# Kernel optimization log

Hardware: AMD Instinct MI355X
Metric: run time of the kernel (lower is better)

The kernel has to match this reference:

```python
import jax, jax.numpy as jnp
import numpy as np

D, K, B, IMG, NCH = 128, 512, 8, 128, 3


def adder2d(x, w, k, stride, pad):
    # AdderNet L1 'convolution': y[b,co,l] = -sum_p |patch[b,p,l] - w[co,p]|
    # x: [B,C,H,W], w: [Cout, C*k*k]
    p = jax.lax.conv_general_dilated_patches(x, (k, k), (stride, stride), [(pad, pad), (pad, pad)])
    Bb, P, Ho, Wo = p.shape
    p = p.reshape(Bb, P, Ho * Wo)  # [B, C*k*k, L]
    def one(wc):  # wc: [P] -> [B, L]; sequential over Cout to bound memory
        return -jnp.sum(jnp.abs(p - wc[None, :, None]), axis=1)
    o = jax.lax.map(one, w)  # [Cout, B, L]
    return jnp.transpose(o, (1, 0, 2)).reshape(Bb, w.shape[0], Ho, Wo)


def bn(x, g, b, eps=1e-5):
    # eval-mode BatchNorm2d with running_mean=0, running_var=1
    s = g * jax.lax.rsqrt(jnp.asarray(1.0 + eps, x.dtype))
    return x * s[None, :, None, None] + b[None, :, None, None]


def conv2d(x, w, b, pad):
    y = jax.lax.conv_general_dilated(x, w, (1, 1), [(pad, pad), (pad, pad)],
                                     dimension_numbers=('NCHW', 'OIHW', 'NCHW'))
    return y + b[None, :, None, None]


def up2x(x):  # nn.Upsample(scale_factor=2, bilinear, align_corners=False)
    Bb, C, H, W = x.shape
    return jax.image.resize(x, (Bb, C, 2 * H, 2 * W), method='bilinear')


def adder_resblock(x, w1, w2, g, b):
    # [ReLU, adder3x3, BN, ReLU, adder1x1] + residual
    h = jax.nn.relu(x)
    h = adder2d(h, w1, 3, 1, 1)
    h = bn(h, g, b)
    h = jax.nn.relu(h)
    h = adder2d(h, w2, 1, 1, 0)
    return x + h


def conv_resblock(x, w1, b1, w2, b2):
    # [ReLU, conv3x3, ReLU, conv1x1] + residual (bn=False in decoder)
    h = jax.nn.relu(x)
    h = conv2d(h, w1, b1, 1)
    h = jax.nn.relu(h)
    h = conv2d(h, w2, b2, 0)
    return x + h


def vq_forward(z_e, E):
    # NearestEmbed: E is [d, k]
    Bb, C, H, W = z_e.shape
    flat = jnp.transpose(z_e, (0, 2, 3, 1)).reshape(-1, C)  # [N, d]
    d2 = (jnp.sum(flat * flat, axis=1, keepdims=True)
          - 2.0 * (flat @ E) + jnp.sum(E * E, axis=0)[None, :])  # [N, k]
    argmin = jnp.argmin(d2, axis=1)  # [N]
    q = jnp.take(E.T, argmin, axis=0)  # [N, d]
    # weight_sg=True path: straight-through to z_e, no grad to E
    zq_flat = flat + jax.lax.stop_gradient(q - flat)
    z_q = jnp.transpose(zq_flat.reshape(Bb, H, W, C), (0, 3, 1, 2))
    # emb path: z_e detached, grad flows to E through the gather
    emb = jnp.transpose(q.reshape(Bb, H, W, C), (0, 3, 1, 2))
    return z_q, emb, argmin.reshape(Bb, H, W)


def reference(x, we1, we2, ae1_w1, ae1_w2, ae2_w1, ae2_w2, bn_gamma, bn_beta,
              emb_weight, rd1_w1, rd1_b1, rd1_w2, rd1_b2, rd2_w1, rd2_b1,
              rd2_w2, rd2_b2, cd1_w, cd1_b, cd2_w, cd2_b):
    g, b = bn_gamma, bn_beta
    h = adder2d(x, we1, 4, 2, 1)
    h = jax.nn.relu(bn(h, g[0], b[0]))
    h = adder2d(h, we2, 4, 2, 1)
    h = jax.nn.relu(bn(h, g[1], b[1]))
    h = adder_resblock(h, ae1_w1, ae1_w2, g[2], b[2])
    h = bn(h, g[3], b[3])
    h = adder_resblock(h, ae2_w1, ae2_w2, g[4], b[4])
    z_e = bn(h, g[5], b[5])  # bne4 (gamma = 1/40)

    z_q, emb, argmin = vq_forward(z_e, emb_weight)

    y = conv_resblock(z_q, rd1_w1, rd1_b1, rd1_w2, rd1_b2)
    y = bn(y, g[6], b[6])
    y = conv_resblock(y, rd2_w1, rd2_b1, rd2_w2, rd2_b2)
    y = up2x(y)
    y = conv2d(y, cd1_w, cd1_b, 1)
    y = jax.nn.relu(bn(y, g[7], b[7]))
    y = up2x(y)
    y = conv2d(y, cd2_w, cd2_b, 1)
    y = jnp.tanh(y)
    return (y, z_e, emb, argmin)


def setup_inputs() -> dict:
    key = jax.random.key(0)
    ks = jax.random.split(key, 16)
    f = lambda k, shp: (0.02 * jax.random.normal(k, shp)).astype(jnp.float32)
    inp = {}
    inp['x'] = jax.random.normal(ks[0], (B, NCH, IMG, IMG), jnp.float32)
    inp['we1'] = f(ks[1], (D, NCH * 16))       # adder 4x4 s2
    inp['we2'] = f(ks[2], (D, D * 16))
    inp['ae1_w1'] = f(ks[3], (D, D * 9))       # adder 3x3
    inp['ae1_w2'] = f(ks[4], (D, D))           # adder 1x1
    inp['ae2_w1'] = f(ks[5], (D, D * 9))
    inp['ae2_w2'] = f(ks[6], (D, D))
    inp['bn_gamma'] = jnp.ones((8, D), jnp.float32).at[5].set(1.0 / 40.0)
    inp['bn_beta'] = jnp.zeros((8, D), jnp.float32)
    inp['emb_weight'] = f(ks[7], (D, K))
    inp['rd1_w1'] = f(ks[8], (D, D, 3, 3)); inp['rd1_b1'] = jnp.zeros(D, jnp.float32)
    inp['rd1_w2'] = f(ks[9], (D, D, 1, 1)); inp['rd1_b2'] = jnp.zeros(D, jnp.float32)
    inp['rd2_w1'] = f(ks[10], (D, D, 3, 3)); inp['rd2_b1'] = jnp.zeros(D, jnp.float32)
    inp['rd2_w2'] = f(ks[11], (D, D, 1, 1)); inp['rd2_b2'] = jnp.zeros(D, jnp.float32)
    inp['cd1_w'] = f(ks[12], (D, D, 3, 3)); inp['cd1_b'] = jnp.zeros(D, jnp.float32)
    inp['cd2_w'] = f(ks[13], (NCH, D, 3, 3)); inp['cd2_b'] = jnp.zeros(NCH, jnp.float32)
    return inp
```

## Files before the change

kernel.cpp:

```cpp
#include <hip/hip_runtime.h>
#include <math.h>

constexpr int Dc = 128;
constexpr int Kc = 512;
constexpr int Bc = 8;

template<int ISADD, int K, int STRIDE, int PAD, int IT, int EPI, int CIN, int CH,
         int PW, int OUT_ROWS, int WOUT, int WIN, int HIN, int HOUT, int COBW,
         int NW, int KSPLIT>
__global__ __launch_bounds__(NW * 64)
void lds_layer(const float* __restrict__ x, const float* __restrict__ w,
               const float* __restrict__ bias,
               const float* __restrict__ itG, const float* __restrict__ itB,
               const float* __restrict__ res,
               const float* __restrict__ rG, const float* __restrict__ rB,
               const float* __restrict__ oG, const float* __restrict__ oB,
               float* __restrict__ out) {
  constexpr int BT = NW * 64;
  constexpr int NWG = NW / KSPLIT;
  constexpr int CINW = CIN / KSPLIT;
  constexpr int CHS = KSPLIT * CH;
  constexpr int KK = K * K;
  constexpr int SPAN = (PW - 1) * STRIDE + K;
  constexpr int IN_ROWS = (OUT_ROWS - 1) * STRIDE + K;
  constexpr int WPAD = (WOUT - 1) * STRIDE + K;
  constexpr int WLDS = (WPAD + 3) & ~3;
  constexpr int PGW = WOUT / PW;
  static_assert(OUT_ROWS * PGW == 64, "one wave covers the pixel tile");
  static_assert(NW % KSPLIT == 0 && CIN % KSPLIT == 0 && CINW % CH == 0, "split");
  static_assert(KSPLIT == 1 ||
                NWG * 64 * PW * COBW <= CHS * IN_ROWS * WLDS, "scratch fits");
  constexpr int NBAND = HOUT / OUT_ROWS;
  constexpr int W4 = WIN / 4;
  constexpr int NELEM4 = CHS * IN_ROWS * W4;
  constexpr int NIT4 = (NELEM4 + BT - 1) / BT;
  constexpr bool EXACT = (NELEM4 % BT) == 0;
  const float r15 = rsqrtf(1.0f + 1e-5f);

  __shared__ alignas(16) float lds[CHS][IN_ROWS][WLDS];

  int tid = threadIdx.x;
  int gb = blockIdx.x;
  int cg = gb / (Bc * NBAND);
  int rem = gb % (Bc * NBAND);
  int band = rem % NBAND;
  int b = rem / NBAND;
  int wv = __builtin_amdgcn_readfirstlane(tid >> 6);
  int lane = tid & 63;
  int grp = wv / NWG;
  int wloc = wv % NWG;
  int co0 = cg * (NWG * COBW) + wloc * COBW;
  int pr = lane / PGW, pc = lane % PGW;
  int oh = band * OUT_ROWS + pr;
  int ow0 = pc * PW;
  int yi0 = band * OUT_ROWS * STRIDE - PAD;

  for (int e = tid; e < CHS * IN_ROWS * WLDS; e += BT) ((float*)lds)[e] = 0.f;

  float acc[PW][COBW];
#pragma unroll
  for (int p = 0; p < PW; ++p)
#pragma unroll
    for (int j = 0; j < COBW; ++j)
      acc[p][j] = (ISADD || grp != 0) ? 0.f : bias[co0 + j];

  const float* xb = x + (long)b * CIN * HIN * WIN;
  float4 rbuf[NIT4];

  auto stage = [&](int cc) {
#pragma unroll
    for (int it = 0; it < NIT4; ++it) {
      int e = it * BT + tid;
      if (!EXACT && e >= NELEM4) break;
      int c4 = e % W4;
      int r = (e / W4) % IN_ROWS;
      int ch2 = e / (W4 * IN_ROWS);
      int gc = cc + (ch2 % CH) + (ch2 / CH) * CINW;
      int yi = yi0 + r;
      float4 v = make_float4(0.f, 0.f, 0.f, 0.f);
      if (yi >= 0 && yi < HIN) {
        v = *(const float4*)&xb[((long)gc * HIN + yi) * WIN + 4 * c4];
        if (IT == 1) {
          v.x = fmaxf(v.x, 0.f); v.y = fmaxf(v.y, 0.f);
          v.z = fmaxf(v.z, 0.f); v.w = fmaxf(v.w, 0.f);
        }
        if (IT == 2) {
          float sc = itG[gc] * r15, bc = itB[gc];
          v.x = fmaxf(fmaf(v.x, sc, bc), 0.f);
          v.y = fmaxf(fmaf(v.y, sc, bc), 0.f);
          v.z = fmaxf(fmaf(v.z, sc, bc), 0.f);
          v.w = fmaxf(fmaf(v.w, sc, bc), 0.f);
        }
      }
      rbuf[it] = v;
    }
  };
  auto towrite = [&]() {
#pragma unroll
    for (int it = 0; it < NIT4; ++it) {
      int e = it * BT + tid;
      if (!EXACT && e >= NELEM4) break;
      int c4 = e % W4;
      int r = (e / W4) % IN_ROWS;
      int ch2 = e / (W4 * IN_ROWS);
      float* p = &lds[ch2][r][4 * c4 + PAD];
      float4 v = rbuf[it];
      p[0] = v.x; p[1] = v.y; p[2] = v.z; p[3] = v.w;
    }
  };

  stage(0);
  for (int cc = 0; cc < CINW; cc += CH) {
    __syncthreads();
    towrite();
    __syncthreads();
    if (cc + CH < CINW) stage(cc + CH);
    for (int chl = 0; chl < CH; ++chl) {
      float vbuf[K][SPAN];
#pragma unroll
      for (int kh = 0; kh < K; ++kh) {
        const float* rp0 = &lds[grp * CH + chl][pr * STRIDE + kh][ow0 * STRIDE];
        if constexpr (SPAN == 6 && (PW * STRIDE) % 4 == 0) {
          float4 a = *(const float4*)rp0;
          float2 c2 = *(const float2*)(rp0 + 4);
          vbuf[kh][0] = a.x; vbuf[kh][1] = a.y; vbuf[kh][2] = a.z;
          vbuf[kh][3] = a.w; vbuf[kh][4] = c2.x; vbuf[kh][5] = c2.y;
        } else if constexpr (SPAN == 4 && (PW * STRIDE) % 2 == 0) {
          float2 a = *(const float2*)rp0;
          float2 c2 = *(const float2*)(rp0 + 2);
          vbuf[kh][0] = a.x; vbuf[kh][1] = a.y;
          vbuf[kh][2] = c2.x; vbuf[kh][3] = c2.y;
        } else if constexpr (SPAN == 2 && (PW * STRIDE) % 2 == 0) {
          float2 a = *(const float2*)rp0;
          vbuf[kh][0] = a.x; vbuf[kh][1] = a.y;
        } else {
#pragma unroll
          for (int s = 0; s < SPAN; ++s) vbuf[kh][s] = rp0[s];
        }
      }
      const float* wc = w + ((long)co0 * CIN + (grp * CINW + cc + chl)) * KK;
#pragma unroll
      for (int kh = 0; kh < K; ++kh)
#pragma unroll
        for (int kw = 0; kw < K; ++kw)
#pragma unroll
          for (int j = 0; j < COBW; ++j) {
            float ww = wc[(long)j * CIN * KK + kh * K + kw];
#pragma unroll
            for (int p = 0; p < PW; ++p) {
              float v = vbuf[kh][p * STRIDE + kw];
              if (ISADD) acc[p][j] += fabsf(v - ww);
              else       acc[p][j] = fmaf(v, ww, acc[p][j]);
            }
          }
    }
  }

  if constexpr (KSPLIT >= 2) {
    float* scr = (float*)lds;
    int sb = (wloc * 64 + lane) * (PW * COBW);
#pragma unroll
    for (int g = 1; g < KSPLIT; ++g) {
      __syncthreads();
      if (grp == g) {
#pragma unroll
        for (int p = 0; p < PW; ++p)
#pragma unroll
          for (int j = 0; j < COBW; ++j) scr[sb + p * COBW + j] = acc[p][j];
      }
      __syncthreads();
      if (grp == 0) {
#pragma unroll
        for (int p = 0; p < PW; ++p)
#pragma unroll
          for (int j = 0; j < COBW; ++j) acc[p][j] += scr[sb + p * COBW + j];
      }
    }
    if (grp != 0) return;
  }

  long obase = ((long)(b * Dc + co0) * HOUT + oh) * WOUT + ow0;
  float* ob = out + obase;
  const float* rp = (EPI == 2 || EPI == 3 || EPI == 6) ? res + obase : nullptr;
  constexpr long hw = (long)HOUT * WOUT;
#pragma unroll
  for (int j = 0; j < COBW; ++j) {
    float og = 0.f, obb = 0.f, rg = 0.f, rbb = 0.f;
    if (EPI == 1 || EPI == 6) { og = oG[co0 + j] * r15; obb = oB[co0 + j]; }
    if (EPI == 3 || EPI == 6) { rg = rG[co0 + j] * r15; rbb = rB[co0 + j]; }
#pragma unroll
    for (int p = 0; p < PW; ++p) {
      float val = ISADD ? -acc[p][j] : acc[p][j];
      if (EPI == 1) val = fmaxf(fmaf(val, og, obb), 0.f);
      if (EPI == 2) val = rp[j * hw + p] + val;
      if (EPI == 3) val = fmaf(rp[j * hw + p], rg, rbb) + val;
      if (EPI == 5) val = fmaxf(val, 0.f);
      if (EPI == 6) val = fmaf(fmaf(rp[j * hw + p], rg, rbb) + val, og, obb);
      ob[j * hw + p] = val;
    }
  }
}

template<int ISADD, int EPI, int COBW>
__global__ __launch_bounds__(256)
void pw1x1(const float* __restrict__ x, const float* __restrict__ w,
           const float* __restrict__ bias,
           const float* __restrict__ res,
           const float* __restrict__ rG, const float* __restrict__ rB,
           const float* __restrict__ oG, const float* __restrict__ oB,
           float* __restrict__ out) {
  constexpr int HW = 1024;
  constexpr int CIN = Dc;
  constexpr int KS = 4;
  constexpr int CSEG = CIN / KS;
  constexpr int PXB = 128;
  constexpr int NPG = HW / PXB;
  constexpr int OPT = (PXB * COBW) / 256;
  static_assert(OPT * 256 == PXB * COBW, "combine exact");
  const float r15 = rsqrtf(1.0f + 1e-5f);

  __shared__ float scr[KS][COBW][PXB];

  int tid = threadIdx.x;
  int wv = __builtin_amdgcn_readfirstlane(tid >> 6);
  int lane = tid & 63;
  int gb = blockIdx.x;
  int cg = gb / (Bc * NPG);
  int rem = gb % (Bc * NPG);
  int pg = rem % NPG;
  int b = rem / NPG;
  int co0 = cg * COBW;
  int px = pg * PXB + lane * 2;

  const float* xc = x + ((long)b * CIN + wv * CSEG) * HW + px;
  const float* wseg = w + wv * CSEG;

  float acc[2][COBW];
#pragma unroll
  for (int p = 0; p < 2; ++p)
#pragma unroll
    for (int j = 0; j < COBW; ++j) acc[p][j] = 0.f;

#pragma unroll 4
  for (int c = 0; c < CSEG; ++c) {
    float2 v = *(const float2*)&xc[(long)c * HW];
#pragma unroll
    for (int j = 0; j < COBW; ++j) {
      float ww = wseg[(long)(co0 + j) * CIN + c];
      if (ISADD) {
        acc[0][j] += fabsf(v.x - ww);
        acc[1][j] += fabsf(v.y - ww);
      } else {
        acc[0][j] = fmaf(v.x, ww, acc[0][j]);
        acc[1][j] = fmaf(v.y, ww, acc[1][j]);
      }
    }
  }

#pragma unroll
  for (int j = 0; j < COBW; ++j) {
    float2 t = make_float2(acc[0][j], acc[1][j]);
    *(float2*)&scr[wv][j][lane * 2] = t;
  }
  __syncthreads();

#pragma unroll
  for (int k = 0; k < OPT; ++k) {
    int e = k * 256 + tid;
    int pxl = e % PXB;
    int j = e / PXB;
    float s = scr[0][j][pxl] + scr[1][j][pxl] + scr[2][j][pxl] + scr[3][j][pxl];
    float val = ISADD ? -s : s + bias[co0 + j];
    long oidx = ((long)b * Dc + co0 + j) * HW + pg * PXB + pxl;
    if (EPI == 2) val = res[oidx] + val;
    if (EPI == 3) {
      float rg = rG[co0 + j] * r15, rbb = rB[co0 + j];
      val = fmaf(res[oidx], rg, rbb) + val;
    }
    if (EPI == 6) {
      float rg = rG[co0 + j] * r15, rbb = rB[co0 + j];
      float og = oG[co0 + j] * r15, obb = oB[co0 + j];
      val = fmaf(fmaf(res[oidx], rg, rbb) + val, og, obb);
    }
    out[oidx] = val;
  }
}

__device__ __forceinline__ void up_coef(int p, int H, int& i0, int& i1, float& w0, float& w1) {
  int m = p >> 1;
  if ((p & 1) == 0) { i0 = (m > 0) ? m - 1 : 0; i1 = m; w0 = 0.25f; w1 = 0.75f; }
  else              { i0 = m; i1 = (m + 1 < H) ? m + 1 : H - 1; w0 = 0.75f; w1 = 0.25f; }
}

__global__ void up2x_kernel(const float* __restrict__ in, float* __restrict__ out,
                            int C, int H, int W) {
  int H2 = 2 * H, W2 = 2 * W;
  int i = blockIdx.x * blockDim.x + threadIdx.x;
  int total = Bc * C * H2 * W2;
  if (i >= total) return;
  int ow = i % W2; int t = i / W2;
  int oh = t % H2; t /= H2;
  int c = t % C; int b = t / C;
  int y0, y1, x0, x1; float wy0, wy1, wx0, wx1;
  up_coef(oh, H, y0, y1, wy0, wy1);
  up_coef(ow, W, x0, x1, wx0, wx1);
  const float* p = in + (b * C + c) * H * W;
  float v = wy0 * (wx0 * p[y0 * W + x0] + wx1 * p[y0 * W + x1])
          + wy1 * (wx0 * p[y1 * W + x0] + wx1 * p[y1 * W + x1]);
  out[i] = v;
}

__global__ __launch_bounds__(256)
void conv3x3_up_tanh_quad(const float* __restrict__ x, const float* __restrict__ w,
                          const float* __restrict__ bias, float* __restrict__ out,
                          int Hs, int Ws, int Cout) {
  constexpr int CIN = Dc;
  int H2 = 2 * Hs, W2 = 2 * Ws;
  int nq = Hs * Ws;
  int i = blockIdx.x * blockDim.x + threadIdx.x;
  int total = Bc * Cout * nq;
  if (i >= total) return;
  int q = i % nq; int t = i / nq;
  int co = t % Cout; int b = t / Cout;
  int n = q % Ws, m = q / Ws;
  int rows[3] = { (m > 0) ? m - 1 : 0, m, (m + 1 < Hs) ? m + 1 : Hs - 1 };
  int cols[3] = { (n > 0) ? n - 1 : 0, n, (n + 1 < Ws) ? n + 1 : Ws - 1 };
  float rv[4] = { (2 * m - 1 >= 0) ? 1.f : 0.f, 1.f, 1.f, (2 * m + 2 < H2) ? 1.f : 0.f };
  float cv[4] = { (2 * n - 1 >= 0) ? 1.f : 0.f, 1.f, 1.f, (2 * n + 2 < W2) ? 1.f : 0.f };
  float bco = bias[co];
  float acc[4] = { bco, bco, bco, bco };
  const float* xb = x + b * CIN * nq;
  const float* wb = w + co * CIN * 9;
  for (int c = 0; c < CIN; ++c) {
    const float* xc = xb + c * nq;
    float s[3][3];
#pragma unroll
    for (int a = 0; a < 3; ++a)
#pragma unroll
      for (int e = 0; e < 3; ++e) s[a][e] = xc[rows[a] * Ws + cols[e]];
    float rb[4][3];
#pragma unroll
    for (int e = 0; e < 3; ++e) {
      rb[0][e] = fmaf(0.75f, s[0][e], 0.25f * s[1][e]);
      rb[1][e] = fmaf(0.25f, s[0][e], 0.75f * s[1][e]);
      rb[2][e] = fmaf(0.75f, s[1][e], 0.25f * s[2][e]);
      rb[3][e] = fmaf(0.25f, s[1][e], 0.75f * s[2][e]);
    }
    float u[4][4];
#pragma unroll
    for (int di = 0; di < 4; ++di) {
      float rm = rv[di];
      u[di][0] = fmaf(0.75f, rb[di][0], 0.25f * rb[di][1]) * rm * cv[0];
      u[di][1] = fmaf(0.25f, rb[di][0], 0.75f * rb[di][1]) * rm * cv[1];
      u[di][2] = fmaf(0.75f, rb[di][1], 0.25f * rb[di][2]) * rm * cv[2];
      u[di][3] = fmaf(0.25f, rb[di][1], 0.75f * rb[di][2]) * rm * cv[3];
    }
    const float* wc = wb + c * 9;
#pragma unroll
    for (int kh = 0; kh < 3; ++kh)
#pragma unroll
      for (int kw = 0; kw < 3; ++kw) {
        float ww = wc[kh * 3 + kw];
        acc[0] = fmaf(u[kh][kw],         ww, acc[0]);
        acc[1] = fmaf(u[kh][kw + 1],     ww, acc[1]);
        acc[2] = fmaf(u[kh + 1][kw],     ww, acc[2]);
        acc[3] = fmaf(u[kh + 1][kw + 1], ww, acc[3]);
      }
  }
  float* ob = out + (b * Cout + co) * H2 * W2 + (2 * m) * W2 + 2 * n;
  ob[0] = tanhf(acc[0]);      ob[1] = tanhf(acc[1]);
  ob[W2] = tanhf(acc[2]);     ob[W2 + 1] = tanhf(acc[3]);
}

__global__ __launch_bounds__(256)
void vq_kernel8(const float* __restrict__ z_e, const float* __restrict__ E,
                float* __restrict__ emb, float* __restrict__ argmin_out) {
  constexpr int HW = 1024;
  __shared__ alignas(16) float f[8][Dc];
  __shared__ float d2s[8][256];
  __shared__ int   ks[8][256];
  int tid = threadIdx.x;
  int n0 = blockIdx.x * 8;
  int b = n0 >> 10;
  int rem = n0 & 1023;
  const float* zb = z_e + (long)b * Dc * HW + rem;
#pragma unroll
  for (int i = 0; i < 4; ++i) {
    int e = i * 256 + tid;
    int p = e & 7, d = e >> 3;
    f[p][d] = zb[d * HW + p];
  }
  __syncthreads();
  float f2 = 0.f;
  if (tid < 8) {
    for (int d = 0; d < Dc; ++d) f2 += f[tid][d] * f[tid][d];
    d2s[tid][0] = f2;
  }
  __syncthreads();
  float f2v[8];
#pragma unroll
  for (int p = 0; p < 8; ++p) f2v[p] = d2s[p][0];
  __syncthreads();

  float best[8]; int bk[8];
#pragma unroll
  for (int p = 0; p < 8; ++p) { best[p] = 3.4e38f; bk[p] = 0; }
  for (int kk = tid; kk < Kc; kk += 256) {
    float dot[8];
#pragma unroll
    for (int p = 0; p < 8; ++p) dot[p] = 0.f;
    float e2k = 0.f;
    for (int d4 = 0; d4 < Dc; d4 += 4) {
      float e0 = E[(long)(d4 + 0) * Kc + kk];
      float e1 = E[(long)(d4 + 1) * Kc + kk];
      float e2c = E[(long)(d4 + 2) * Kc + kk];
      float e3 = E[(long)(d4 + 3) * Kc + kk];
      e2k = fmaf(e0, e0, e2k);
      e2k = fmaf(e1, e1, e2k);
      e2k = fmaf(e2c, e2c, e2k);
      e2k = fmaf(e3, e3, e2k);
#pragma unroll
      for (int p = 0; p < 8; ++p) {
        float4 fv = *(const float4*)&f[p][d4];
        dot[p] = fmaf(fv.x, e0, dot[p]);
        dot[p] = fmaf(fv.y, e1, dot[p]);
        dot[p] = fmaf(fv.z, e2c, dot[p]);
        dot[p] = fmaf(fv.w, e3, dot[p]);
      }
    }
#pragma unroll
    for (int p = 0; p < 8; ++p) {
      float d2 = f2v[p] - 2.f * dot[p] + e2k;
      if (d2 < best[p] || (d2 == best[p] && kk < bk[p])) { best[p] = d2; bk[p] = kk; }
    }
  }
#pragma unroll
  for (int p = 0; p < 8; ++p) { d2s[p][tid] = best[p]; ks[p][tid] = bk[p]; }
  __syncthreads();
  for (int s = 128; s > 0; s >>= 1) {
    if (tid < s) {
#pragma unroll
      for (int p = 0; p < 8; ++p) {
        float ob = d2s[p][tid + s]; int ok = ks[p][tid + s];
        if (ob < d2s[p][tid] || (ob == d2s[p][tid] && ok < ks[p][tid])) {
          d2s[p][tid] = ob; ks[p][tid] = ok;
        }
      }
    }
    __syncthreads();
  }
  if (tid < 8) argmin_out[n0 + tid] = (float)ks[tid][0];
  float* eb = emb + (long)b * Dc * HW + rem;
#pragma unroll
  for (int i = 0; i < 4; ++i) {
    int e = i * 256 + tid;
    int p = e & 7, d = e >> 3;
    eb[d * HW + p] = E[d * Kc + ks[p][0]];
  }
}

extern "C" void kernel_launch(void* const* d_in, const int* in_sizes, int n_in,
                              void* d_out, int out_size, void* d_ws, size_t ws_size,
                              hipStream_t stream) {
  const float* x      = (const float*)d_in[0];
  const float* we1    = (const float*)d_in[1];
  const float* we2    = (const float*)d_in[2];
  const float* ae1_w1 = (const float*)d_in[3];
  const float* ae1_w2 = (const float*)d_in[4];
  const float* ae2_w1 = (const float*)d_in[5];
  const float* ae2_w2 = (const float*)d_in[6];
  const float* bn_g   = (const float*)d_in[7];
  const float* bn_b   = (const float*)d_in[8];
  const float* embw   = (const float*)d_in[9];
  const float* rd1_w1 = (const float*)d_in[10];
  const float* rd1_b1 = (const float*)d_in[11];
  const float* rd1_w2 = (const float*)d_in[12];
  const float* rd1_b2 = (const float*)d_in[13];
  const float* rd2_w1 = (const float*)d_in[14];
  const float* rd2_b1 = (const float*)d_in[15];
  const float* rd2_w2 = (const float*)d_in[16];
  const float* rd2_b2 = (const float*)d_in[17];
  const float* cd1_w  = (const float*)d_in[18];
  const float* cd1_b  = (const float*)d_in[19];
  const float* cd2_w  = (const float*)d_in[20];
  const float* cd2_b  = (const float*)d_in[21];

  const float* g0 = bn_g + 0 * Dc; const float* b0 = bn_b + 0 * Dc;
  const float* g1 = bn_g + 1 * Dc; const float* b1 = bn_b + 1 * Dc;
  const float* g2 = bn_g + 2 * Dc; const float* b2 = bn_b + 2 * Dc;
  const float* g3 = bn_g + 3 * Dc; const float* b3 = bn_b + 3 * Dc;
  const float* g4 = bn_g + 4 * Dc; const float* b4 = bn_b + 4 * Dc;
  const float* g5 = bn_g + 5 * Dc; const float* b5 = bn_b + 5 * Dc;
  const float* g6 = bn_g + 6 * Dc; const float* b6 = bn_b + 6 * Dc;
  const float* g7 = bn_g + 7 * Dc; const float* b7 = bn_b + 7 * Dc;

  float* W64a = (float*)d_ws;
  float* W64b = W64a + 4194304;
  float* Wa   = W64b + 4194304;
  float* Wb   = Wa + 1048576;
  float* Wc   = Wb + 1048576;

  float* out_y   = (float*)d_out;
  float* out_ze  = out_y  + 393216;
  float* out_emb = out_ze + 1048576;
  float* out_am  = out_emb + 1048576;

  const int TB = 256;
  const int TB8 = 512;
  auto nb = [](int n) { return (n + 255) / 256; };
  const int N64 = Bc * Dc * 64 * 64;
  const float* nul = nullptr;

  const int G32s = 16 * Bc * 8;
  const int Gwe1 = 8 * Bc * 32;
  const int Gcd1 = 4 * Bc * 32;
  const int Gpw  = 32 * Bc * 8;

  lds_layer<1,4,2,1, 0,1, 3,3, 2, 2,64,128,128,64, 4,4,1><<<Gwe1, TB, 0, stream>>>(
      x, we1, nul, nul, nul, nul, nul, nul, g0, b0, W64a);
  lds_layer<1,4,2,1, 0,1, Dc,4, 2, 4,32,64,64,32, 2,8,2><<<G32s, TB8, 0, stream>>>(
      W64a, we2, nul, nul, nul, nul, nul, nul, g1, b1, Wa);
  lds_layer<1,3,1,1, 0,1, Dc,16, 2, 4,32,32,32,32, 2,8,2><<<G32s, TB8, 0, stream>>>(
      Wa, ae1_w1, nul, nul, nul, nul, nul, nul, g2, b2, Wb);
  pw1x1<1,2,4><<<Gpw, TB, 0, stream>>>(
      Wb, ae1_w2, nul, Wa, nul, nul, nul, nul, Wc);
  lds_layer<1,3,1,1, 2,1, Dc,16, 2, 4,32,32,32,32, 2,8,2><<<G32s, TB8, 0, stream>>>(
      Wc, ae2_w1, nul, g3, b3, nul, nul, nul, g4, b4, Wb);
  pw1x1<1,6,4><<<Gpw, TB, 0, stream>>>(
      Wb, ae2_w2, nul, Wc, g3, b3, g5, b5, out_ze);

  vq_kernel8<<<Bc * 1024 / 8, 256, 0, stream>>>(out_ze, embw, out_emb, out_am);

  lds_layer<0,3,1,1, 1,5, Dc,16, 2, 4,32,32,32,32, 2,8,2><<<G32s, TB8, 0, stream>>>(
      out_emb, rd1_w1, rd1_b1, nul, nul, nul, nul, nul, nul, nul, Wb);
  pw1x1<0,2,4><<<Gpw, TB, 0, stream>>>(
      Wb, rd1_w2, rd1_b2, out_emb, nul, nul, nul, nul, Wa);
  lds_layer<0,3,1,1, 2,5, Dc,16, 2, 4,32,32,32,32, 2,8,2><<<G32s, TB8, 0, stream>>>(
      Wa, rd2_w1, rd2_b1, g6, b6, nul, nul, nul, nul, nul, Wb);
  pw1x1<0,3,4><<<Gpw, TB, 0, stream>>>(
      Wb, rd2_w2, rd2_b2, Wa, g6, b6, nul, nul, Wc);

  up2x_kernel<<<nb(N64), TB, 0, stream>>>(Wc, W64a, Dc, 32, 32);
  lds_layer<0,3,1,1, 0,1, Dc,8, 2, 2,64,64,64,64, 8,8,2><<<Gcd1, TB8, 0, stream>>>(
      W64a, cd1_w, cd1_b, nul, nul, nul, nul, nul, g7, b7, W64b);

  conv3x3_up_tanh_quad<<<nb(Bc * 3 * 64 * 64), TB, 0, stream>>>(W64b, cd2_w, cd2_b, out_y, 64, 64, 3);
}
```

Before: 828.2 us.

## Split final upsample-conv input channels across warps and reduce via LDS

The final 3x3 conv fused with bilinear upsample and tanh now splits the 128 input channels into 4 segments, one per wavefront of a 256-thread block. Partial sums are reduced through shared memory, and each thread then writes one output pixel. This multiplies the available parallelism for a small kernel (3 output channels) at the cost of an LDS reduction and a barrier. It also adds a `#pragma unroll 2` on the per-channel loop of the generic LDS layer kernel.

```diff
diff --git a/kernel.cpp b/kernel.cpp
--- a/kernel.cpp
+++ b/kernel.cpp
@@ -115,6 +115,7 @@
     towrite();
     __syncthreads();
     if (cc + CH < CINW) stage(cc + CH);
+#pragma unroll 2
     for (int chl = 0; chl < CH; ++chl) {
       float vbuf[K][SPAN];
 #pragma unroll
@@ -311,27 +312,32 @@
 }
 
 __global__ __launch_bounds__(256)
-void conv3x3_up_tanh_quad(const float* __restrict__ x, const float* __restrict__ w,
-                          const float* __restrict__ bias, float* __restrict__ out,
-                          int Hs, int Ws, int Cout) {
+void conv3x3_up_tanh_ks(const float* __restrict__ x, const float* __restrict__ w,
+                        const float* __restrict__ bias, float* __restrict__ out,
+                        int Hs, int Ws, int Cout) {
   constexpr int CIN = Dc;
+  constexpr int SEG = 4;
+  constexpr int CSEG = CIN / SEG;
+  constexpr int QB = 64;
+  __shared__ float scr[SEG][4][QB];
+
   int H2 = 2 * Hs, W2 = 2 * Ws;
   int nq = Hs * Ws;
-  int i = blockIdx.x * blockDim.x + threadIdx.x;
-  int total = Bc * Cout * nq;
-  if (i >= total) return;
-  int q = i % nq; int t = i / nq;
-  int co = t % Cout; int b = t / Cout;
+  int tid = threadIdx.x;
+  int q_l = tid % QB;
+  int seg = tid / QB;
+  int gq = blockIdx.x * QB + q_l;
+  int q = gq % nq; int t2 = gq / nq;
+  int co = t2 % Cout; int b = t2 / Cout;
   int n = q % Ws, m = q / Ws;
   int rows[3] = { (m > 0) ? m - 1 : 0, m, (m + 1 < Hs) ? m + 1 : Hs - 1 };
   int cols[3] = { (n > 0) ? n - 1 : 0, n, (n + 1 < Ws) ? n + 1 : Ws - 1 };
   float rv[4] = { (2 * m - 1 >= 0) ? 1.f : 0.f, 1.f, 1.f, (2 * m + 2 < H2) ? 1.f : 0.f };
   float cv[4] = { (2 * n - 1 >= 0) ? 1.f : 0.f, 1.f, 1.f, (2 * n + 2 < W2) ? 1.f : 0.f };
-  float bco = bias[co];
-  float acc[4] = { bco, bco, bco, bco };
-  const float* xb = x + b * CIN * nq;
-  const float* wb = w + co * CIN * 9;
-  for (int c = 0; c < CIN; ++c) {
+  float acc[4] = { 0.f, 0.f, 0.f, 0.f };
+  const float* xb = x + (b * CIN + seg * CSEG) * nq;
+  const float* wb = w + (co * CIN + seg * CSEG) * 9;
+  for (int c = 0; c < CSEG; ++c) {
     const float* xc = xb + c * nq;
     float s[3][3];
 #pragma unroll
@@ -367,9 +373,14 @@
         acc[3] = fmaf(u[kh + 1][kw + 1], ww, acc[3]);
       }
   }
-  float* ob = out + (b * Cout + co) * H2 * W2 + (2 * m) * W2 + 2 * n;
-  ob[0] = tanhf(acc[0]);      ob[1] = tanhf(acc[1]);
-  ob[W2] = tanhf(acc[2]);     ob[W2 + 1] = tanhf(acc[3]);
+#pragma unroll
+  for (int di = 0; di < 4; ++di) scr[seg][di][q_l] = acc[di];
+  __syncthreads();
+  int di = tid / QB;
+  float sum = scr[0][di][q_l] + scr[1][di][q_l] + scr[2][di][q_l]
+            + scr[3][di][q_l] + bias[co];
+  out[(long)(b * Cout + co) * H2 * W2 + (2 * m + (di >> 1)) * W2 + 2 * n + (di & 1)]
+      = tanhf(sum);
 }
 
 __global__ __launch_bounds__(256)
@@ -515,6 +526,7 @@
   const int Gwe1 = 8 * Bc * 32;
   const int Gcd1 = 4 * Bc * 32;
   const int Gpw  = 32 * Bc * 8;
+  const int Gct  = Bc * 3 * 64 * 64 / 64;
 
   lds_layer<1,4,2,1, 0,1, 3,3, 2, 2,64,128,128,64, 4,4,1><<<Gwe1, TB, 0, stream>>>(
       x, we1, nul, nul, nul, nul, nul, nul, g0, b0, W64a);
@@ -544,5 +556,5 @@
   lds_layer<0,3,1,1, 0,1, Dc,8, 2, 2,64,64,64,64, 8,8,2><<<Gcd1, TB8, 0, stream>>>(
       W64a, cd1_w, cd1_b, nul, nul, nul, nul, nul, g7, b7, W64b);
 
-  conv3x3_up_tanh_quad<<<nb(Bc * 3 * 64 * 64), TB, 0, stream>>>(W64b, cd2_w, cd2_b, out_y, 64, 64, 3);
-}
+  conv3x3_up_tanh_ks<<<Gct, TB, 0, stream>>>(W64b, cd2_w, cd2_b, out_y, 64, 64, 3);
+}
```

New measurement: 783.7 us. 1.06x faster.
